# Performance work log

Hardware: AMD Instinct MI355X
Metric: run time of the kernel (lower is better)

## Reference

```python
import jax, jax.numpy as jnp
import numpy as np

EPS = 1e-5
TOP_K = 2


def setup_inputs() -> dict:
    key = jax.random.key(0)
    ks = jax.random.split(key, 8)
    B, T, D, E, F = 4, 2048, 1024, 8, 4096
    s_in = 1.0 / np.sqrt(D)
    s_ff = 1.0 / np.sqrt(F)
    return {
        "hidden_states": jax.random.normal(ks[0], (B, T, D), jnp.float32),
        "input_tensor": jax.random.normal(ks[1], (B, T, D), jnp.float32),
        "gate_w": jax.random.normal(ks[2], (D, E), jnp.float32) * s_in,
        "gate_b": jnp.zeros((E,), jnp.float32),
        "w1": jax.random.normal(ks[3], (E, D, F), jnp.float32) * s_in,
        "b1": jnp.zeros((E, F), jnp.float32),
        "w2": jax.random.normal(ks[4], (E, F, D), jnp.float32) * s_ff,
        "b2": jnp.zeros((E, D), jnp.float32),
        "gamma": jnp.ones((D,), jnp.float32),
        "beta": jnp.zeros((D,), jnp.float32),
    }


def _layer_norm(x, gamma, beta):
    mu = jnp.mean(x, axis=-1, keepdims=True)
    var = jnp.mean(jnp.square(x - mu), axis=-1, keepdims=True)
    return (x - mu) * jax.lax.rsqrt(var + EPS) * gamma + beta


def reference(hidden_states, input_tensor, gate_w, gate_b, w1, b1, w2, b2, gamma, beta):
    E = gate_b.shape[0]
    # Router: softmax over experts, then top-k gate values/indices.
    gate_logits = jnp.einsum("btd,de->bte", hidden_states, gate_w) + gate_b
    gate_probs = jax.nn.softmax(gate_logits, axis=-1)
    topk_gates, topk_idx = jax.lax.top_k(gate_probs, TOP_K)  # [B,T,K]
    # Combine weights per expert: sum of top-k gate values routed to expert e.
    combine_w = jnp.sum(
        jax.nn.one_hot(topk_idx, E, dtype=hidden_states.dtype)
        * topk_gates[..., None],
        axis=-2,
    )  # [B,T,E]
    # Dispatch/combine: weighted sum of expert FFN outputs (loop over small fixed E).
    expert_outputs = jnp.zeros_like(hidden_states)
    for e in range(E):
        h = jax.nn.gelu(jnp.einsum("btd,df->btf", hidden_states, w1[e]) + b1[e])
        y = jnp.einsum("btf,fd->btd", h, w2[e]) + b2[e]
        expert_outputs = expert_outputs + combine_w[..., e:e + 1] * y
    # Dropout is identity in eval mode.
    return _layer_norm(expert_outputs + input_tensor, gamma, beta)
```

## Files before the change

kernel.cpp:

```cpp
#include <hip/hip_runtime.h>

#define TOKENS 8192
#define DIM 1024
#define NEXP 8
#define FDIM 4096

typedef __bf16 bf16x8 __attribute__((ext_vector_type(8)));
typedef float f32x4 __attribute__((ext_vector_type(4)));

__device__ __forceinline__ unsigned short f2bf(float f) {
  unsigned u = __builtin_bit_cast(unsigned, f);
  u += 0x7fffu + ((u >> 16) & 1u);
  return (unsigned short)(u >> 16);
}

__device__ __forceinline__ float bf2f(unsigned short s) {
  unsigned u = (unsigned)s << 16;
  return __builtin_bit_cast(float, u);
}

__device__ __forceinline__ void gload16(const void* g, void* l) {
  __builtin_amdgcn_global_load_lds(
      (const __attribute__((address_space(1))) unsigned int*)g,
      (__attribute__((address_space(3))) unsigned int*)l, 16, 0, 0);
}

__global__ void zero_counts_kernel(int* counts) {
  if (threadIdx.x < NEXP) counts[threadIdx.x] = 0;
}

__global__ void scan_kernel(const int* counts, int* offs, int* nchk,
                            int* chunks0, int* chunks1) {
  if (threadIdx.x == 0) {
    int s = 0;
    for (int e = 0; e < NEXP; ++e) { offs[e] = s; s += counts[e]; }
    offs[NEXP] = s;
    int nc0 = 0, nc1 = 0;
    for (int e = 0; e < NEXP; ++e) {
      const int mt = (counts[e] + 255) >> 8;
      for (int mc = 0; mc < mt; mc += 4) {
        for (int n4 = 0; n4 < 16; n4 += 4)
          chunks0[nc0++] = (e << 16) | (mc << 8) | n4;
        chunks1[nc1++] = (e << 16) | (mc << 8);
      }
    }
    nchk[0] = nc0;
    nchk[1] = nc1;
  }
}

__global__ void router_kernel(const float* __restrict__ hs,
                              const float* __restrict__ gw,
                              const float* __restrict__ gb,
                              int* __restrict__ counts,
                              int* __restrict__ tok_idx,
                              float* __restrict__ tok_w,
                              unsigned int* __restrict__ slotinfo,
                              unsigned short* __restrict__ hs_bf) {
  const int lane = threadIdx.x & 63;
  const int wid = threadIdx.x >> 6;
  const int t = blockIdx.x * 4 + wid;
  const float* row = hs + (size_t)t * DIM;

  float x[16];
  const float4* r4 = (const float4*)(row + lane * 16);
#pragma unroll
  for (int i = 0; i < 4; ++i) {
    float4 v = r4[i];
    x[i * 4 + 0] = v.x; x[i * 4 + 1] = v.y; x[i * 4 + 2] = v.z; x[i * 4 + 3] = v.w;
  }

  float acc[8];
#pragma unroll
  for (int e = 0; e < 8; ++e) acc[e] = 0.f;
#pragma unroll
  for (int i = 0; i < 16; ++i) {
    const int d = lane * 16 + i;
    const float4* g4 = (const float4*)(gw + (size_t)d * 8);
    float4 g0 = g4[0], g1 = g4[1];
    const float xv = x[i];
    acc[0] += xv * g0.x; acc[1] += xv * g0.y; acc[2] += xv * g0.z; acc[3] += xv * g0.w;
    acc[4] += xv * g1.x; acc[5] += xv * g1.y; acc[6] += xv * g1.z; acc[7] += xv * g1.w;
  }
#pragma unroll
  for (int sh = 1; sh < 64; sh <<= 1) {
#pragma unroll
    for (int e = 0; e < 8; ++e) acc[e] += __shfl_xor(acc[e], sh, 64);
  }
#pragma unroll
  for (int e = 0; e < 8; ++e) acc[e] += gb[e];

  float mx = acc[0];
#pragma unroll
  for (int e = 1; e < 8; ++e) mx = fmaxf(mx, acc[e]);
  float p[8];
  float sum = 0.f;
#pragma unroll
  for (int e = 0; e < 8; ++e) { p[e] = __expf(acc[e] - mx); sum += p[e]; }
  const float inv = 1.0f / sum;

  int i0 = 0; float b0 = p[0];
#pragma unroll
  for (int e = 1; e < 8; ++e) if (p[e] > b0) { b0 = p[e]; i0 = e; }
  int i1 = -1; float b1v = -1.f;
#pragma unroll
  for (int e = 0; e < 8; ++e) if (e != i0 && p[e] > b1v) { b1v = p[e]; i1 = e; }

  if (lane == 0) {
    int pos0 = atomicAdd(&counts[i0], 1);
    tok_idx[i0 * TOKENS + pos0] = t;
    tok_w[i0 * TOKENS + pos0] = b0 * inv;
    int pos1 = atomicAdd(&counts[i1], 1);
    tok_idx[i1 * TOKENS + pos1] = t;
    tok_w[i1 * TOKENS + pos1] = b1v * inv;
    slotinfo[t] = ((unsigned)i0 << 29) | ((unsigned)pos0 << 16) |
                  ((unsigned)i1 << 13) | (unsigned)pos1;
  }

  unsigned short us[16];
#pragma unroll
  for (int i = 0; i < 16; ++i) us[i] = f2bf(x[i]);
  uint4 o0, o1;
  o0.x = (unsigned)us[0] | ((unsigned)us[1] << 16);
  o0.y = (unsigned)us[2] | ((unsigned)us[3] << 16);
  o0.z = (unsigned)us[4] | ((unsigned)us[5] << 16);
  o0.w = (unsigned)us[6] | ((unsigned)us[7] << 16);
  o1.x = (unsigned)us[8] | ((unsigned)us[9] << 16);
  o1.y = (unsigned)us[10] | ((unsigned)us[11] << 16);
  o1.z = (unsigned)us[12] | ((unsigned)us[13] << 16);
  o1.w = (unsigned)us[14] | ((unsigned)us[15] << 16);
  uint4* dst = (uint4*)(hs_bf + (size_t)t * DIM + lane * 16);
  dst[0] = o0;
  dst[1] = o1;
}

__global__ void cast_transpose_all(const float* __restrict__ w1,
                                   unsigned short* __restrict__ w1t,
                                   const float* __restrict__ w2,
                                   unsigned short* __restrict__ w2t) {
  __shared__ float tile[64][65];
  const int L = blockIdx.x;
  const float* src;
  unsigned short* dstp;
  int R, C, bi;
  if (L < 8192) { src = w1; dstp = w1t; R = DIM;  C = FDIM; bi = L; }
  else          { src = w2; dstp = w2t; R = FDIM; C = DIM;  bi = L - 8192; }
  const int nx = C >> 6;
  const int e = bi >> 10;
  const int w = bi & 1023;
  const int by = w / nx, bx = w % nx;
  const int r0 = by * 64, c0 = bx * 64;
  const float* s = src + (size_t)e * R * C;
  unsigned int* d = (unsigned int*)(dstp + (size_t)e * R * C);

#pragma unroll
  for (int i = 0; i < 16; ++i) {
    const int idx = threadIdx.x + i * 256;
    const int r = idx >> 6;
    const int c = idx & 63;
    tile[r][c] = s[(size_t)(r0 + r) * C + (c0 + c)];
  }
  __syncthreads();
#pragma unroll
  for (int i = 0; i < 8; ++i) {
    const int idx = threadIdx.x + i * 256;
    const int c = idx >> 5;
    const int r = (idx & 31) * 2;
    unsigned pk = (unsigned)f2bf(tile[r][c]) | ((unsigned)f2bf(tile[r + 1][c]) << 16);
    d[((size_t)(c0 + c) * R + (r0 + r)) >> 1] = pk;
  }
}


#define MOE_STEP(DB, NB, DOST, G1STR, DOG2)                                          \
  {                                                                                  \
    bf16x8 af_[4], bf_[4];                                                           \
                                                            \
    _Pragma("unroll") for (int f_ = 0; f_ < 4; ++f_)                                 \
      af_[f_] = *(const bf16x8*)(smc + (DB) + aoff[f_]);                             \
    _Pragma("unroll") for (int g_ = 0; g_ < 4; ++g_)                                 \
      bf_[g_] = *(const bf16x8*)(smc + (DB) + 32768 + boff[g_]);                     \
    if (DOST) { gload16(aS0, smw + (NB)); gload16(aS1, smw + (NB) + 8192); }         \
    __builtin_amdgcn_sched_barrier(0);                                               \
    __builtin_amdgcn_s_barrier();                                                    \
    asm volatile("s_waitcnt lgkmcnt(0)" ::: "memory");                               \
    __builtin_amdgcn_sched_barrier(0);                                               \
    __builtin_amdgcn_s_setprio(1);                                                   \
    _Pragma("unroll") for (int f_ = 0; f_ < 4; ++f_)                                 \
      _Pragma("unroll") for (int g_ = 0; g_ < 4; ++g_)                               \
        acc[f_][g_] = __builtin_amdgcn_mfma_f32_16x16x32_bf16(af_[f_], bf_[g_],      \
                                                              acc[f_][g_], 0, 0, 0); \
    __builtin_amdgcn_s_setprio(0);                                                   \
    __builtin_amdgcn_sched_barrier(0);                                               \
    __builtin_amdgcn_s_barrier();                                                    \
                                                            \
    _Pragma("unroll") for (int f_ = 0; f_ < 4; ++f_)                                 \
      af_[f_] = *(const bf16x8*)(smc + (DB) + aoff[4 + f_]);                         \
    if (DOST) { gload16(bS0, smw + (NB) + 32768); gload16(bS1, smw + (NB) + 40960); }\
    __builtin_amdgcn_sched_barrier(0);                                               \
    __builtin_amdgcn_s_barrier();                                                    \
    asm volatile("s_waitcnt lgkmcnt(0)" ::: "memory");                               \
    __builtin_amdgcn_sched_barrier(0);                                               \
    __builtin_amdgcn_s_setprio(1);                                                   \
    _Pragma("unroll") for (int f_ = 0; f_ < 4; ++f_)                                 \
      _Pragma("unroll") for (int g_ = 0; g_ < 4; ++g_)                               \
        acc[4 + f_][g_] = __builtin_amdgcn_mfma_f32_16x16x32_bf16(af_[f_], bf_[g_],  \
                                                          acc[4 + f_][g_], 0, 0, 0); \
    __builtin_amdgcn_s_setprio(0);                                                   \
    __builtin_amdgcn_sched_barrier(0);                                               \
    asm volatile(G1STR ::: "memory");                                                \
    __builtin_amdgcn_s_barrier();                                                    \
                                                            \
    _Pragma("unroll") for (int f_ = 0; f_ < 4; ++f_)                                 \
      af_[f_] = *(const bf16x8*)(smc + (DB) + 16384 + aoff[f_]);                     \
    _Pragma("unroll") for (int g_ = 0; g_ < 4; ++g_)                                 \
      bf_[g_] = *(const bf16x8*)(smc + (DB) + 49152 + boff[g_]);                     \
    if (DOST) { gload16(aS0 + 64, smw + (NB) + 16384);                               \
                gload16(aS1 + 64, smw + (NB) + 24576); }                             \
    __builtin_amdgcn_sched_barrier(0);                                               \
    __builtin_amdgcn_s_barrier();                                                    \
    asm volatile("s_waitcnt lgkmcnt(0)" ::: "memory");                               \
    __builtin_amdgcn_sched_barrier(0);                                               \
    __builtin_amdgcn_s_setprio(1);                                                   \
    _Pragma("unroll") for (int f_ = 0; f_ < 4; ++f_)                                 \
      _Pragma("unroll") for (int g_ = 0; g_ < 4; ++g_)                               \
        acc[f_][g_] = __builtin_amdgcn_mfma_f32_16x16x32_bf16(af_[f_], bf_[g_],      \
                                                              acc[f_][g_], 0, 0, 0); \
    __builtin_amdgcn_s_setprio(0);                                                   \
    __builtin_amdgcn_sched_barrier(0);                                               \
    __builtin_amdgcn_s_barrier();                                                    \
                                                            \
    _Pragma("unroll") for (int f_ = 0; f_ < 4; ++f_)                                 \
      af_[f_] = *(const bf16x8*)(smc + (DB) + 16384 + aoff[4 + f_]);                 \
    if (DOST) { gload16(bS0 + 64, smw + (NB) + 49152);                               \
                gload16(bS1 + 64, smw + (NB) + 57344);                               \
                aS0 += 128; aS1 += 128; bS0 += 128; bS1 += 128; }                    \
    __builtin_amdgcn_sched_barrier(0);                                               \
    __builtin_amdgcn_s_barrier();                                                    \
    asm volatile("s_waitcnt lgkmcnt(0)" ::: "memory");                               \
    __builtin_amdgcn_sched_barrier(0);                                               \
    __builtin_amdgcn_s_setprio(1);                                                   \
    _Pragma("unroll") for (int f_ = 0; f_ < 4; ++f_)                                 \
      _Pragma("unroll") for (int g_ = 0; g_ < 4; ++g_)                               \
        acc[4 + f_][g_] = __builtin_amdgcn_mfma_f32_16x16x32_bf16(af_[f_], bf_[g_],  \
                                                          acc[4 + f_][g_], 0, 0, 0); \
    __builtin_amdgcn_s_setprio(0);                                                   \
    __builtin_amdgcn_sched_barrier(0);                                               \
    if (DOG2) {                                                                      \
      asm volatile("s_waitcnt vmcnt(4)" ::: "memory");                               \
      __builtin_amdgcn_s_barrier();                                                  \
    }                                                                                \
  }

template<int MODE, int K, int N>
__global__ __launch_bounds__(512, 2)
void moe_gemm(const unsigned short* __restrict__ Abase,
              const unsigned short* __restrict__ Bbase,
              const float* __restrict__ bias,
              const int* __restrict__ counts,
              const int* __restrict__ offs,
              const int* __restrict__ tok_idx,
              const int* __restrict__ chunktab,
              const int* __restrict__ nchk,
              unsigned short* __restrict__ dst) {
  constexpr int NS = K / 64;
  __shared__ __align__(16) unsigned char sm[131072];

  const int L = blockIdx.x;
  const int xk = L & 7;
  const int tt = L >> 3;
  const int g = (tt >> 4) * 8 + xk;
  if (g >= nchk[MODE]) return;
  const int within = tt & 15;
  const int cd = chunktab[g];
  const int e = cd >> 16;
  const int cnt = counts[e];
  const int m0 = (((cd >> 8) & 255) + (within >> 2)) * 256;
  if (m0 >= cnt) return;
  const int n0 = ((cd & 255) + (within & 3)) * 256;
  const int goff = offs[e];

  const int tid = threadIdx.x;
  const int lane = tid & 63;
  const int wid = tid >> 6;
  const int wr = wid >> 2;
  const int wcn = wid & 3;
  const int l15 = lane & 15;
  const int cg = lane >> 4;
  const int wdst = wid * 1024;

  const int urow = tid >> 2;
  const int uchk = tid & 3;
  const int swz = uchk ^ ((urow >> 1) & 3);
  const unsigned char* Bexp = (const unsigned char*)(Bbase + (size_t)e * K * N);

  int gA0 = m0 + urow;       if (gA0 > cnt - 1) gA0 = cnt - 1;
  int gA1 = m0 + urow + 128; if (gA1 > cnt - 1) gA1 = cnt - 1;
  size_t rowA0, rowA1;
  if (MODE == 0) {
    rowA0 = (size_t)tok_idx[e * TOKENS + gA0] * K;
    rowA1 = (size_t)tok_idx[e * TOKENS + gA1] * K;
  } else {
    rowA0 = (size_t)(goff + gA0) * K;
    rowA1 = (size_t)(goff + gA1) * K;
  }
  const unsigned char* aS0 = (const unsigned char*)(Abase + rowA0) + swz * 16;
  const unsigned char* aS1 = (const unsigned char*)(Abase + rowA1) + swz * 16;
  const unsigned char* bS0 = Bexp + (size_t)(n0 + urow) * (K * 2) + swz * 16;
  const unsigned char* bS1 = Bexp + (size_t)(n0 + urow + 128) * (K * 2) + swz * 16;

  int aoff[8], boff[4];
#pragma unroll
  for (int f = 0; f < 8; ++f) {
    const int r = wr * 128 + f * 16 + l15;
    aoff[f] = r * 64 + ((cg ^ ((r >> 1) & 3)) * 16);
  }
#pragma unroll
  for (int g2 = 0; g2 < 4; ++g2) {
    const int r = wcn * 64 + g2 * 16 + l15;
    boff[g2] = r * 64 + ((cg ^ ((r >> 1) & 3)) * 16);
  }

  f32x4 acc[8][4];
  const f32x4 fz = {0.f, 0.f, 0.f, 0.f};
#pragma unroll
  for (int f = 0; f < 8; ++f)
#pragma unroll
    for (int g2 = 0; g2 < 4; ++g2) acc[f][g2] = fz;

  const unsigned char* smc = (const unsigned char*)sm;
  unsigned char* smw = (unsigned char*)sm + wdst;

  gload16(aS0, smw);                gload16(aS1, smw + 8192);
  gload16(bS0, smw + 32768);        gload16(bS1, smw + 40960);
  gload16(aS0 + 64, smw + 16384);   gload16(aS1 + 64, smw + 24576);
  gload16(bS0 + 64, smw + 49152);   gload16(bS1 + 64, smw + 57344);
  aS0 += 128; aS1 += 128; bS0 += 128; bS1 += 128;
  asm volatile("s_waitcnt vmcnt(4)" ::: "memory");
  __builtin_amdgcn_sched_barrier(0);
  __builtin_amdgcn_s_barrier();

#pragma unroll 1
  for (int it = 0; it < (NS - 2) / 2; ++it) {
    MOE_STEP(0,     65536, 1, "s_waitcnt vmcnt(4)", 1);
    MOE_STEP(65536, 0,     1, "s_waitcnt vmcnt(4)", 1);
  }
  MOE_STEP(0,     65536, 1, "s_waitcnt vmcnt(4)", 1);
  MOE_STEP(65536, 0,     0, "s_waitcnt vmcnt(0)", 0);

#pragma unroll
  for (int g2 = 0; g2 < 4; ++g2) {
    const int fcol = n0 + wcn * 64 + g2 * 16 + l15;
    const float bv = bias[e * N + fcol];
#pragma unroll
    for (int f = 0; f < 8; ++f) {
#pragma unroll
      for (int j = 0; j < 4; ++j) {
        const int ml = wr * 128 + f * 16 + cg * 4 + j;
        const int gm = m0 + ml;
        if (gm < cnt) {
          float v = acc[f][g2][j] + bv;
          if (MODE == 0) {
            const float u = 0.7978845608028654f * (v + 0.044715f * v * v * v);
            const float th = 1.0f - 2.0f / (1.0f + __expf(2.0f * u));
            v = 0.5f * v * (1.0f + th);
          }
          dst[(size_t)(goff + gm) * N + fcol] = f2bf(v);
        }
      }
    }
  }
}

__global__ void ln_combine_kernel(const unsigned short* __restrict__ y_buf,
                                  const float* __restrict__ in_t,
                                  const int* __restrict__ offs,
                                  const unsigned int* __restrict__ slotinfo,
                                  const float* __restrict__ tok_w,
                                  const float* __restrict__ gamma,
                                  const float* __restrict__ beta,
                                  float* __restrict__ out) {
  const int lane = threadIdx.x & 63;
  const int wid = threadIdx.x >> 6;
  const int t = blockIdx.x * 4 + wid;

  const unsigned s = slotinfo[t];
  const int e0 = s >> 29, p0 = (s >> 16) & 8191;
  const int e1 = (s >> 13) & 7, p1 = s & 8191;
  const float w0 = tok_w[e0 * TOKENS + p0];
  const float w1 = tok_w[e1 * TOKENS + p1];
  const size_t r0 = (size_t)(offs[e0] + p0) * DIM;
  const size_t r1 = (size_t)(offs[e1] + p1) * DIM;

  float v[16];
  {
    const float4* i4 = (const float4*)(in_t + (size_t)t * DIM + lane * 16);
    const uint4* y0 = (const uint4*)(y_buf + r0 + lane * 16);
    const uint4* y1 = (const uint4*)(y_buf + r1 + lane * 16);
#pragma unroll
    for (int i = 0; i < 4; ++i) {
      float4 a = i4[i];
      v[i * 4 + 0] = a.x; v[i * 4 + 1] = a.y; v[i * 4 + 2] = a.z; v[i * 4 + 3] = a.w;
    }
#pragma unroll
    for (int i = 0; i < 2; ++i) {
      uint4 u0 = y0[i];
      uint4 u1 = y1[i];
      const unsigned uw0[4] = {u0.x, u0.y, u0.z, u0.w};
      const unsigned uw1[4] = {u1.x, u1.y, u1.z, u1.w};
#pragma unroll
      for (int k = 0; k < 4; ++k) {
        const int base = i * 8 + k * 2;
        v[base + 0] += w0 * bf2f((unsigned short)(uw0[k] & 0xffff)) +
                       w1 * bf2f((unsigned short)(uw1[k] & 0xffff));
        v[base + 1] += w0 * bf2f((unsigned short)(uw0[k] >> 16)) +
                       w1 * bf2f((unsigned short)(uw1[k] >> 16));
      }
    }
  }

  float sum = 0.f, s2 = 0.f;
#pragma unroll
  for (int i = 0; i < 16; ++i) { sum += v[i]; s2 += v[i] * v[i]; }
#pragma unroll
  for (int sh = 1; sh < 64; sh <<= 1) {
    sum += __shfl_xor(sum, sh, 64);
    s2 += __shfl_xor(s2, sh, 64);
  }
  const float mu = sum * (1.0f / DIM);
  const float var = s2 * (1.0f / DIM) - mu * mu;
  const float rs = rsqrtf(var + 1e-5f);

  float4* w4 = (float4*)(out + (size_t)t * DIM + lane * 16);
#pragma unroll
  for (int i = 0; i < 4; ++i) {
    const int d = lane * 16 + i * 4;
    float4 gg = *(const float4*)(gamma + d);
    float4 bb = *(const float4*)(beta + d);
    float4 o;
    o.x = (v[i * 4 + 0] - mu) * rs * gg.x + bb.x;
    o.y = (v[i * 4 + 1] - mu) * rs * gg.y + bb.y;
    o.z = (v[i * 4 + 2] - mu) * rs * gg.z + bb.z;
    o.w = (v[i * 4 + 3] - mu) * rs * gg.w + bb.w;
    w4[i] = o;
  }
}

extern "C" void kernel_launch(void* const* d_in, const int* in_sizes, int n_in,
                              void* d_out, int out_size, void* d_ws, size_t ws_size,
                              hipStream_t stream) {
  const float* hs    = (const float*)d_in[0];
  const float* in_t  = (const float*)d_in[1];
  const float* gw    = (const float*)d_in[2];
  const float* gb    = (const float*)d_in[3];
  const float* w1    = (const float*)d_in[4];
  const float* b1    = (const float*)d_in[5];
  const float* w2    = (const float*)d_in[6];
  const float* b2    = (const float*)d_in[7];
  const float* gamma = (const float*)d_in[8];
  const float* beta  = (const float*)d_in[9];
  float* out = (float*)d_out;
  char* ws = (char*)d_ws;

  int* counts            = (int*)(ws + 0);
  int* offs              = (int*)(ws + 256);
  unsigned int* slotinfo = (unsigned int*)(ws + 512);
  int* nchk              = (int*)(ws + 33280);
  int* chunks0           = (int*)(ws + 33536);
  int* chunks1           = (int*)(ws + 34048);
  int* tok_idx           = (int*)(ws + 66048);
  float* tok_w           = (float*)(ws + 328192);
  unsigned short* hs_bf  = (unsigned short*)(ws + 590336);
  unsigned short* w1t    = (unsigned short*)(ws + 17367552);
  unsigned short* w2t    = (unsigned short*)(ws + 84476416);
  unsigned short* h_buf  = (unsigned short*)(ws + 151585280);
  unsigned short* y_buf  = (unsigned short*)(ws + 590336);

  zero_counts_kernel<<<1, 64, 0, stream>>>(counts);
  router_kernel<<<TOKENS / 4, 256, 0, stream>>>(hs, gw, gb, counts, tok_idx, tok_w,
                                                slotinfo, hs_bf);
  scan_kernel<<<1, 64, 0, stream>>>(counts, offs, nchk, chunks0, chunks1);
  cast_transpose_all<<<16384, 256, 0, stream>>>(w1, w1t, w2, w2t);
  moe_gemm<0, DIM, FDIM><<<1536, 512, 0, stream>>>(
      hs_bf, w1t, b1, counts, offs, tok_idx, chunks0, nchk, h_buf);
  moe_gemm<1, FDIM, DIM><<<384, 512, 0, stream>>>(
      h_buf, w2t, b2, counts, offs, tok_idx, chunks1, nchk, y_buf);
  ln_combine_kernel<<<TOKENS / 4, 256, 0, stream>>>(y_buf, in_t, offs, slotinfo,
                                                    tok_w, gamma, beta, out);
}
```

Baseline: 796.8 us.

## Replace 256x256 pipelined MoE GEMM with simple 128x128 single-buffered tiles

Drops the hand-scheduled double-buffered 256x256 GEMM macro and uses 128x128 tiles with 256-thread blocks, 32KB LDS and a plain load/sync/compute loop. The chunk tables and grid sizes are rescaled to match. The smaller tiles give more blocks and better occupancy, and waste less padding on ragged expert counts. In exchange they lose the software pipelining and have lower arithmetic intensity per tile.

```diff
diff --git a/kernel.cpp b/kernel.cpp
--- a/kernel.cpp
+++ b/kernel.cpp
@@ -37,11 +37,12 @@
     offs[NEXP] = s;
     int nc0 = 0, nc1 = 0;
     for (int e = 0; e < NEXP; ++e) {
-      const int mt = (counts[e] + 255) >> 8;
+      const int mt = (counts[e] + 127) >> 7;
       for (int mc = 0; mc < mt; mc += 4) {
-        for (int n4 = 0; n4 < 16; n4 += 4)
+        for (int n4 = 0; n4 < 32; n4 += 4)
           chunks0[nc0++] = (e << 16) | (mc << 8) | n4;
-        chunks1[nc1++] = (e << 16) | (mc << 8);
+        for (int n4 = 0; n4 < 8; n4 += 4)
+          chunks1[nc1++] = (e << 16) | (mc << 8) | n4;
       }
     }
     nchk[0] = nc0;
@@ -171,89 +172,8 @@
   }
 }
 
-
-#define MOE_STEP(DB, NB, DOST, G1STR, DOG2)                                          \
-  {                                                                                  \
-    bf16x8 af_[4], bf_[4];                                                           \
-                                                            \
-    _Pragma("unroll") for (int f_ = 0; f_ < 4; ++f_)                                 \
-      af_[f_] = *(const bf16x8*)(smc + (DB) + aoff[f_]);                             \
-    _Pragma("unroll") for (int g_ = 0; g_ < 4; ++g_)                                 \
-      bf_[g_] = *(const bf16x8*)(smc + (DB) + 32768 + boff[g_]);                     \
-    if (DOST) { gload16(aS0, smw + (NB)); gload16(aS1, smw + (NB) + 8192); }         \
-    __builtin_amdgcn_sched_barrier(0);                                               \
-    __builtin_amdgcn_s_barrier();                                                    \
-    asm volatile("s_waitcnt lgkmcnt(0)" ::: "memory");                               \
-    __builtin_amdgcn_sched_barrier(0);                                               \
-    __builtin_amdgcn_s_setprio(1);                                                   \
-    _Pragma("unroll") for (int f_ = 0; f_ < 4; ++f_)                                 \
-      _Pragma("unroll") for (int g_ = 0; g_ < 4; ++g_)                               \
-        acc[f_][g_] = __builtin_amdgcn_mfma_f32_16x16x32_bf16(af_[f_], bf_[g_],      \
-                                                              acc[f_][g_], 0, 0, 0); \
-    __builtin_amdgcn_s_setprio(0);                                                   \
-    __builtin_amdgcn_sched_barrier(0);                                               \
-    __builtin_amdgcn_s_barrier();                                                    \
-                                                            \
-    _Pragma("unroll") for (int f_ = 0; f_ < 4; ++f_)                                 \
-      af_[f_] = *(const bf16x8*)(smc + (DB) + aoff[4 + f_]);                         \
-    if (DOST) { gload16(bS0, smw + (NB) + 32768); gload16(bS1, smw + (NB) + 40960); }\
-    __builtin_amdgcn_sched_barrier(0);                                               \
-    __builtin_amdgcn_s_barrier();                                                    \
-    asm volatile("s_waitcnt lgkmcnt(0)" ::: "memory");                               \
-    __builtin_amdgcn_sched_barrier(0);                                               \
-    __builtin_amdgcn_s_setprio(1);                                                   \
-    _Pragma("unroll") for (int f_ = 0; f_ < 4; ++f_)                                 \
-      _Pragma("unroll") for (int g_ = 0; g_ < 4; ++g_)                               \
-        acc[4 + f_][g_] = __builtin_amdgcn_mfma_f32_16x16x32_bf16(af_[f_], bf_[g_],  \
-                                                          acc[4 + f_][g_], 0, 0, 0); \
-    __builtin_amdgcn_s_setprio(0);                                                   \
-    __builtin_amdgcn_sched_barrier(0);                                               \
-    asm volatile(G1STR ::: "memory");                                                \
-    __builtin_amdgcn_s_barrier();                                                    \
-                                                            \
-    _Pragma("unroll") for (int f_ = 0; f_ < 4; ++f_)                                 \
-      af_[f_] = *(const bf16x8*)(smc + (DB) + 16384 + aoff[f_]);                     \
-    _Pragma("unroll") for (int g_ = 0; g_ < 4; ++g_)                                 \
-      bf_[g_] = *(const bf16x8*)(smc + (DB) + 49152 + boff[g_]);                     \
-    if (DOST) { gload16(aS0 + 64, smw + (NB) + 16384);                               \
-                gload16(aS1 + 64, smw + (NB) + 24576); }                             \
-    __builtin_amdgcn_sched_barrier(0);                                               \
-    __builtin_amdgcn_s_barrier();                                                    \
-    asm volatile("s_waitcnt lgkmcnt(0)" ::: "memory");                               \
-    __builtin_amdgcn_sched_barrier(0);                                               \
-    __builtin_amdgcn_s_setprio(1);                                                   \
-    _Pragma("unroll") for (int f_ = 0; f_ < 4; ++f_)                                 \
-      _Pragma("unroll") for (int g_ = 0; g_ < 4; ++g_)                               \
-        acc[f_][g_] = __builtin_amdgcn_mfma_f32_16x16x32_bf16(af_[f_], bf_[g_],      \
-                                                              acc[f_][g_], 0, 0, 0); \
-    __builtin_amdgcn_s_setprio(0);                                                   \
-    __builtin_amdgcn_sched_barrier(0);                                               \
-    __builtin_amdgcn_s_barrier();                                                    \
-                                                            \
-    _Pragma("unroll") for (int f_ = 0; f_ < 4; ++f_)                                 \
-      af_[f_] = *(const bf16x8*)(smc + (DB) + 16384 + aoff[4 + f_]);                 \
-    if (DOST) { gload16(bS0 + 64, smw + (NB) + 49152);                               \
-                gload16(bS1 + 64, smw + (NB) + 57344);                               \
-                aS0 += 128; aS1 += 128; bS0 += 128; bS1 += 128; }                    \
-    __builtin_amdgcn_sched_barrier(0);                                               \
-    __builtin_amdgcn_s_barrier();                                                    \
-    asm volatile("s_waitcnt lgkmcnt(0)" ::: "memory");                               \
-    __builtin_amdgcn_sched_barrier(0);                                               \
-    __builtin_amdgcn_s_setprio(1);                                                   \
-    _Pragma("unroll") for (int f_ = 0; f_ < 4; ++f_)                                 \
-      _Pragma("unroll") for (int g_ = 0; g_ < 4; ++g_)                               \
-        acc[4 + f_][g_] = __builtin_amdgcn_mfma_f32_16x16x32_bf16(af_[f_], bf_[g_],  \
-                                                          acc[4 + f_][g_], 0, 0, 0); \
-    __builtin_amdgcn_s_setprio(0);                                                   \
-    __builtin_amdgcn_sched_barrier(0);                                               \
-    if (DOG2) {                                                                      \
-      asm volatile("s_waitcnt vmcnt(4)" ::: "memory");                               \
-      __builtin_amdgcn_s_barrier();                                                  \
-    }                                                                                \
-  }
-
 template<int MODE, int K, int N>
-__global__ __launch_bounds__(512, 2)
+__global__ __launch_bounds__(256, 4)
 void moe_gemm(const unsigned short* __restrict__ Abase,
               const unsigned short* __restrict__ Bbase,
               const float* __restrict__ bias,
@@ -264,7 +184,7 @@
               const int* __restrict__ nchk,
               unsigned short* __restrict__ dst) {
   constexpr int NS = K / 64;
-  __shared__ __align__(16) unsigned char sm[131072];
+  __shared__ __align__(16) unsigned char sm[32768];
 
   const int L = blockIdx.x;
   const int xk = L & 7;
@@ -275,27 +195,25 @@
   const int cd = chunktab[g];
   const int e = cd >> 16;
   const int cnt = counts[e];
-  const int m0 = (((cd >> 8) & 255) + (within >> 2)) * 256;
+  const int m0 = (((cd >> 8) & 255) + (within >> 2)) * 128;
   if (m0 >= cnt) return;
-  const int n0 = ((cd & 255) + (within & 3)) * 256;
+  const int n0 = ((cd & 255) + (within & 3)) * 128;
   const int goff = offs[e];
 
   const int tid = threadIdx.x;
   const int lane = tid & 63;
   const int wid = tid >> 6;
-  const int wr = wid >> 2;
-  const int wcn = wid & 3;
+  const int wm = wid >> 1;
+  const int wn = wid & 1;
   const int l15 = lane & 15;
   const int cg = lane >> 4;
-  const int wdst = wid * 1024;
-
-  const int urow = tid >> 2;
-  const int uchk = tid & 3;
-  const int swz = uchk ^ ((urow >> 1) & 3);
+
+  const int trow = tid >> 2;
+  const int tswz = (tid & 3) ^ ((trow >> 1) & 3);
   const unsigned char* Bexp = (const unsigned char*)(Bbase + (size_t)e * K * N);
 
-  int gA0 = m0 + urow;       if (gA0 > cnt - 1) gA0 = cnt - 1;
-  int gA1 = m0 + urow + 128; if (gA1 > cnt - 1) gA1 = cnt - 1;
+  int gA0 = m0 + trow;      if (gA0 > cnt - 1) gA0 = cnt - 1;
+  int gA1 = m0 + trow + 64; if (gA1 > cnt - 1) gA1 = cnt - 1;
   size_t rowA0, rowA1;
   if (MODE == 0) {
     rowA0 = (size_t)tok_idx[e * TOKENS + gA0] * K;
@@ -304,59 +222,64 @@
     rowA0 = (size_t)(goff + gA0) * K;
     rowA1 = (size_t)(goff + gA1) * K;
   }
-  const unsigned char* aS0 = (const unsigned char*)(Abase + rowA0) + swz * 16;
-  const unsigned char* aS1 = (const unsigned char*)(Abase + rowA1) + swz * 16;
-  const unsigned char* bS0 = Bexp + (size_t)(n0 + urow) * (K * 2) + swz * 16;
-  const unsigned char* bS1 = Bexp + (size_t)(n0 + urow + 128) * (K * 2) + swz * 16;
-
-  int aoff[8], boff[4];
-#pragma unroll
-  for (int f = 0; f < 8; ++f) {
-    const int r = wr * 128 + f * 16 + l15;
-    aoff[f] = r * 64 + ((cg ^ ((r >> 1) & 3)) * 16);
-  }
+  const unsigned char* pA0 = (const unsigned char*)(Abase + rowA0) + tswz * 16;
+  const unsigned char* pA1 = (const unsigned char*)(Abase + rowA1) + tswz * 16;
+  const unsigned char* pB0 = Bexp + (size_t)(n0 + trow) * (K * 2) + tswz * 16;
+  const unsigned char* pB1 = Bexp + (size_t)(n0 + trow + 64) * (K * 2) + tswz * 16;
+
+  const int swc = (cg ^ ((l15 >> 1) & 3)) * 16;
+  const int aB = wm * 4096 + l15 * 64 + swc;
+  const int bB = 16384 + wn * 4096 + l15 * 64 + swc;
+  const unsigned char* smc = (const unsigned char*)sm;
+  unsigned char* smw = (unsigned char*)sm + tid * 16;
+
+  f32x4 acc[4][4];
+  const f32x4 fz = {0.f, 0.f, 0.f, 0.f};
+#pragma unroll
+  for (int f = 0; f < 4; ++f)
+#pragma unroll
+    for (int g2 = 0; g2 < 4; ++g2) acc[f][g2] = fz;
+
+#pragma unroll 1
+  for (int st = 0; st < NS; ++st) {
+    gload16(pA0, smw);
+    gload16(pA1, smw + 4096);
+    gload16(pA0 + 64, smw + 8192);
+    gload16(pA1 + 64, smw + 12288);
+    gload16(pB0, smw + 16384);
+    gload16(pB1, smw + 20480);
+    gload16(pB0 + 64, smw + 24576);
+    gload16(pB1 + 64, smw + 28672);
+    pA0 += 128; pA1 += 128; pB0 += 128; pB1 += 128;
+    __syncthreads();
+#pragma unroll
+    for (int s = 0; s < 2; ++s) {
+      bf16x8 af[4], bfr[4];
+#pragma unroll
+      for (int f = 0; f < 4; ++f)
+        af[f] = *(const bf16x8*)(smc + aB + s * 8192 + f * 1024);
+#pragma unroll
+      for (int g2 = 0; g2 < 4; ++g2)
+        bfr[g2] = *(const bf16x8*)(smc + bB + s * 8192 + g2 * 1024);
+#pragma unroll
+      for (int f = 0; f < 4; ++f)
+#pragma unroll
+        for (int g2 = 0; g2 < 4; ++g2)
+          acc[f][g2] = __builtin_amdgcn_mfma_f32_16x16x32_bf16(af[f], bfr[g2],
+                                                               acc[f][g2], 0, 0, 0);
+    }
+    __syncthreads();
+  }
+
 #pragma unroll
   for (int g2 = 0; g2 < 4; ++g2) {
-    const int r = wcn * 64 + g2 * 16 + l15;
-    boff[g2] = r * 64 + ((cg ^ ((r >> 1) & 3)) * 16);
-  }
-
-  f32x4 acc[8][4];
-  const f32x4 fz = {0.f, 0.f, 0.f, 0.f};
-#pragma unroll
-  for (int f = 0; f < 8; ++f)
-#pragma unroll
-    for (int g2 = 0; g2 < 4; ++g2) acc[f][g2] = fz;
-
-  const unsigned char* smc = (const unsigned char*)sm;
-  unsigned char* smw = (unsigned char*)sm + wdst;
-
-  gload16(aS0, smw);                gload16(aS1, smw + 8192);
-  gload16(bS0, smw + 32768);        gload16(bS1, smw + 40960);
-  gload16(aS0 + 64, smw + 16384);   gload16(aS1 + 64, smw + 24576);
-  gload16(bS0 + 64, smw + 49152);   gload16(bS1 + 64, smw + 57344);
-  aS0 += 128; aS1 += 128; bS0 += 128; bS1 += 128;
-  asm volatile("s_waitcnt vmcnt(4)" ::: "memory");
-  __builtin_amdgcn_sched_barrier(0);
-  __builtin_amdgcn_s_barrier();
-
-#pragma unroll 1
-  for (int it = 0; it < (NS - 2) / 2; ++it) {
-    MOE_STEP(0,     65536, 1, "s_waitcnt vmcnt(4)", 1);
-    MOE_STEP(65536, 0,     1, "s_waitcnt vmcnt(4)", 1);
-  }
-  MOE_STEP(0,     65536, 1, "s_waitcnt vmcnt(4)", 1);
-  MOE_STEP(65536, 0,     0, "s_waitcnt vmcnt(0)", 0);
-
-#pragma unroll
-  for (int g2 = 0; g2 < 4; ++g2) {
-    const int fcol = n0 + wcn * 64 + g2 * 16 + l15;
+    const int fcol = n0 + wn * 64 + g2 * 16 + l15;
     const float bv = bias[e * N + fcol];
 #pragma unroll
-    for (int f = 0; f < 8; ++f) {
+    for (int f = 0; f < 4; ++f) {
 #pragma unroll
       for (int j = 0; j < 4; ++j) {
-        const int ml = wr * 128 + f * 16 + cg * 4 + j;
+        const int ml = wm * 64 + f * 16 + cg * 4 + j;
         const int gm = m0 + ml;
         if (gm < cnt) {
           float v = acc[f][g2][j] + bv;
@@ -467,7 +390,7 @@
   unsigned int* slotinfo = (unsigned int*)(ws + 512);
   int* nchk              = (int*)(ws + 33280);
   int* chunks0           = (int*)(ws + 33536);
-  int* chunks1           = (int*)(ws + 34048);
+  int* chunks1           = (int*)(ws + 35072);
   int* tok_idx           = (int*)(ws + 66048);
   float* tok_w           = (float*)(ws + 328192);
   unsigned short* hs_bf  = (unsigned short*)(ws + 590336);
@@ -481,9 +404,9 @@
                                                 slotinfo, hs_bf);
   scan_kernel<<<1, 64, 0, stream>>>(counts, offs, nchk, chunks0, chunks1);
   cast_transpose_all<<<16384, 256, 0, stream>>>(w1, w1t, w2, w2t);
-  moe_gemm<0, DIM, FDIM><<<1536, 512, 0, stream>>>(
+  moe_gemm<0, DIM, FDIM><<<6144, 256, 0, stream>>>(
       hs_bf, w1t, b1, counts, offs, tok_idx, chunks0, nchk, h_buf);
-  moe_gemm<1, FDIM, DIM><<<384, 512, 0, stream>>>(
+  moe_gemm<1, FDIM, DIM><<<2048, 256, 0, stream>>>(
       h_buf, w2t, b2, counts, offs, tok_idx, chunks1, nchk, y_buf);
   ln_combine_kernel<<<TOKENS / 4, 256, 0, stream>>>(y_buf, in_t, offs, slotinfo,
                                                     tok_w, gamma, beta, out);
```

After: 743.7 us. -6.7%, faster.
